# Kernel tuning notes

Hardware: AMD Instinct MI355X
Metric: run time of the kernel (lower is better)

## Reference

```python
import jax, jax.numpy as jnp
import numpy as np

D_MODEL = 256; D_FFN = 1024; N_LEVELS = 4; N_HEADS = 8; N_POINTS = 4; N_VT = 8
D_HEAD = D_MODEL // N_HEADS
SHAPES = [(64, 64), (32, 32), (16, 16), (8, 8)]
L_SP = sum(h * w for h, w in SHAPES)  # 5440
BATCH = 4
EPS = 1e-5


def _ln(x, g, b):
    m = jnp.mean(x, -1, keepdims=True)
    xc = x - m
    v = jnp.mean(xc * xc, -1, keepdims=True)
    return g * xc * jax.lax.rsqrt(v + EPS) + b


def _bilinear(v_flat, x, y, H, W):
    # v_flat: (N, H*W, M, Dh); x, y: (N, Q, M) pixel coords (align_corners=False, zero padding)
    x0 = jnp.floor(x); y0 = jnp.floor(y)
    wx = x - x0; wy = y - y0
    out = 0.0
    for cx, cy, w in ((x0, y0, (1 - wx) * (1 - wy)), (x0 + 1, y0, wx * (1 - wy)),
                      (x0, y0 + 1, (1 - wx) * wy), (x0 + 1, y0 + 1, wx * wy)):
        valid = (cx >= 0) & (cx < W) & (cy >= 0) & (cy < H)
        xi = jnp.clip(cx, 0, W - 1).astype(jnp.int32)
        yi = jnp.clip(cy, 0, H - 1).astype(jnp.int32)
        idx = (yi * W + xi)[..., None]  # (N, Q, M, 1)
        g = jnp.take_along_axis(v_flat, idx, axis=1)  # (N, Q, M, Dh)
        out = out + (w * valid)[..., None] * g
    return out


def _msdeform_attn(query, ref, value_in, shapes_np, pad_mask, Wv, bv, Wo, bo, Wa, ba, Wp, bp):
    N, Lq, D = query.shape
    M, Lv, P, Dh = N_HEADS, N_LEVELS, N_POINTS, D_HEAD
    value = value_in @ Wv.T + bv
    value = jnp.where(pad_mask[..., None], 0.0, value)
    value = value.reshape(N, Lq, M, Dh)
    off = (query @ Wo.T + bo).reshape(N, Lq, M, Lv, P, 2)
    attn = jax.nn.softmax((query @ Wa.T + ba).reshape(N, Lq, M, Lv * P), axis=-1)
    attn = attn.reshape(N, Lq, M, Lv, P)
    # offset normalizer is (W, H) per level
    normalizer = jnp.asarray([[w, h] for h, w in shapes_np], jnp.float32)
    loc = ref[:, :, None, :, None, :] + off / normalizer[None, None, None, :, None, :]
    out = 0.0
    start = 0
    for l, (H, W) in enumerate(shapes_np):
        v_l = value[:, start:start + H * W]  # (N, H*W, M, Dh)
        x = (loc[:, :, :, l, :, 0] * W - 0.5).transpose(0, 1, 3, 2).reshape(N, Lq * P, M)
        y = (loc[:, :, :, l, :, 1] * H - 0.5).transpose(0, 1, 3, 2).reshape(N, Lq * P, M)
        samp = _bilinear(v_l, x, y, H, W).reshape(N, Lq, P, M, Dh)
        out = out + jnp.einsum('nqpmd,nqmp->nqmd', samp, attn[:, :, :, l, :])
        start += H * W
    return out.reshape(N, Lq, D) @ Wp.T + bp


def setup_inputs() -> dict:
    key = jax.random.key(0)
    ks = jax.random.split(key, 16)
    N, D = BATCH, D_MODEL
    Lq = L_SP + N_VT
    s = D ** -0.5
    rn = lambda k, sh, sc=1.0: jax.random.normal(k, sh, dtype=jnp.float32) * sc
    starts = np.cumsum([0] + [h * w for h, w in SHAPES[:-1]])
    return {
        'src': rn(ks[0], (N, L_SP, D)),
        'pos': rn(ks[1], (N, L_SP, D), 0.1),
        'reference_points': jax.random.uniform(ks[2], (N, Lq, N_LEVELS, 2), dtype=jnp.float32),
        'spatial_shapes': jnp.asarray(SHAPES, jnp.int32),
        'level_start_index': jnp.asarray(starts, jnp.int32),
        'padding_mask': jnp.zeros((N, Lq), bool),
        'all_vt': rn(ks[3], (N, 75 * N_VT, D)),
        'sel_vt': rn(ks[4], (N, N_VT, D)),
        'W_value': rn(ks[5], (D, D), s), 'b_value': jnp.zeros((D,), jnp.float32),
        'W_off': rn(ks[6], (N_HEADS * N_LEVELS * N_POINTS * 2, D), s),
        'b_off': rn(ks[7], (N_HEADS * N_LEVELS * N_POINTS * 2,), 0.1),
        'W_attn': rn(ks[8], (N_HEADS * N_LEVELS * N_POINTS, D), s),
        'b_attn': jnp.zeros((N_HEADS * N_LEVELS * N_POINTS,), jnp.float32),
        'W_out': rn(ks[9], (D, D), s), 'b_out': jnp.zeros((D,), jnp.float32),
        'g1': jnp.ones((D,), jnp.float32), 'beta1': jnp.zeros((D,), jnp.float32),
        'W1': rn(ks[10], (D_FFN, D), s), 'bf1': jnp.zeros((D_FFN,), jnp.float32),
        'W2': rn(ks[11], (D, D_FFN), D_FFN ** -0.5), 'bf2': jnp.zeros((D,), jnp.float32),
        'g2': jnp.ones((D,), jnp.float32), 'beta2': jnp.zeros((D,), jnp.float32),
    }


def reference(src, pos, reference_points, spatial_shapes, level_start_index, padding_mask,
              all_vt, sel_vt, W_value, b_value, W_off, b_off, W_attn, b_attn, W_out, b_out,
              g1, beta1, W1, bf1, W2, bf2, g2, beta2):
    shapes_np = [tuple(int(v) for v in row) for row in np.asarray(spatial_shapes)]
    q = jnp.concatenate([src + pos, sel_vt], axis=1)      # (N, Lq, D)
    v_in = jnp.concatenate([src, sel_vt], axis=1)
    src2 = _msdeform_attn(q, reference_points, v_in, shapes_np, padding_mask,
                          W_value, b_value, W_off, b_off, W_attn, b_attn, W_out, b_out)
    x = _ln(v_in + src2, g1, beta1)
    h = jax.nn.relu(x @ W1.T + bf1) @ W2.T + bf2
    x = _ln(x + h, g2, beta2)
    return (x[:, :L_SP, :], all_vt, x[:, L_SP:, :])
```

## Files before the change

### kernel.cpp

```cpp
#include <hip/hip_runtime.h>
#include <math.h>

#define NB   4
#define LQ   5448
#define LSP  5440
#define NR   21792
#define DM   256

typedef unsigned short u16;
typedef __attribute__((ext_vector_type(8))) short short8;
typedef __attribute__((ext_vector_type(4))) float f32x4;
typedef __attribute__((ext_vector_type(4))) unsigned int uint4v;

__device__ __forceinline__ u16 f2bf(float f) {
  unsigned int u = __float_as_uint(f);
  u = (u + 0x7fff + ((u >> 16) & 1)) >> 16;
  return (u16)u;
}
__device__ __forceinline__ float bf2f(u16 u) {
  return __uint_as_float(((unsigned int)u) << 16);
}
__device__ __forceinline__ uint4v pack8(float4 a, float4 b) {
  uint4v r;
  r.x = (unsigned)f2bf(a.x) | ((unsigned)f2bf(a.y) << 16);
  r.y = (unsigned)f2bf(a.z) | ((unsigned)f2bf(a.w) << 16);
  r.z = (unsigned)f2bf(b.x) | ((unsigned)f2bf(b.y) << 16);
  r.w = (unsigned)f2bf(b.z) | ((unsigned)f2bf(b.w) << 16);
  return r;
}

#define OFF_R0 0ull
#define OFF_R1 44630016ull
#define OFF_R2 55787520ull
#define OFF_R3 66945024ull
#define OFF_WB 78102528ull
#define OFF_BI 79609856ull

#define WOF_V  0
#define WOF_OA 65536
#define WOF_P  163840
#define WOF_1  229376
#define WOF_2  491520
#define NWELEM 753664

#define OUT0 5570560ull
#define OUT1 614400ull

__global__ __launch_bounds__(256) void convw_k(
    const float* __restrict__ Wv, const float* __restrict__ Wo,
    const float* __restrict__ Wa, const float* __restrict__ Wp,
    const float* __restrict__ W1, const float* __restrict__ W2,
    const float* __restrict__ bo, const float* __restrict__ ba,
    u16* __restrict__ out, float* __restrict__ boa)
{
  const int gid = blockIdx.x * 256 + threadIdx.x;
  if (gid < 384) boa[gid] = (gid < 256) ? bo[gid] : ba[gid - 256];
  if (gid >= NWELEM) return;
  float v;
  if (gid < WOF_OA) {
    v = Wv[gid];
  } else if (gid < WOF_P) {
    const int o = gid - WOF_OA;
    v = (o < 65536) ? Wo[o] : Wa[o - 65536];
  } else if (gid < WOF_1) {
    v = Wp[gid - WOF_P];
  } else if (gid < WOF_2) {
    v = W1[gid - WOF_1];
  } else {
    v = W2[gid - WOF_2];
  }
  out[gid] = f2bf(v);
}

template <int AMODE, int EPI, int BN>
__global__ __launch_bounds__(BN) void gemmP(
    const u16* __restrict__ A, int lda,
    const float* __restrict__ src, const float* __restrict__ pos,
    const float* __restrict__ sel,
    const u16* __restrict__ B, int ldb,
    const float* __restrict__ bias, int K,
    u16* __restrict__ outb, int ldob,
    const u16* __restrict__ xbf,
    const float* __restrict__ gvec, const float* __restrict__ bvec,
    float* __restrict__ outf, int ldof)
{
  constexpr int NW = BN / 64;
  __shared__ u16 As[32 * 256];
  __shared__ u16 Bs[NW * 4096];
  const int tid = threadIdx.x;
  const int w = tid >> 6, lane = tid & 63;
  const int l15 = lane & 15, quad = lane >> 4;
  const int m0 = blockIdx.y * 32;
  const int n0 = blockIdx.x * BN;
  const int swz = (quad ^ ((l15 >> 1) & 3)) * 8;

  const int rA = (tid & 127) >> 2;
  const int pA = tid & 3;
  const int jb = ((tid >> 7) & 1) * 4;
  const int cA = (pA ^ ((rA >> 1) & 3)) * 8;
  const int ldsA = rA * 32 + pA * 8;
  int gmA = m0 + rA; if (gmA >= NR) gmA = NR - 1;
  const float* aV = nullptr; const float* aP = nullptr;
  if (AMODE) {
    const int n = gmA / LQ, i = gmA - n * LQ;
    if (i < LSP) {
      aV = src + ((size_t)(n * LSP + i)) * DM;
      if (AMODE == 1) aP = pos + ((size_t)(n * LSP + i)) * DM;
    } else {
      aV = sel + ((size_t)(n * 8 + (i - LSP))) * DM;
    }
  }

  int rB[4], cB[4], lB[4];
#pragma unroll
  for (int i = 0; i < 4; ++i) {
    const int g = lane + i * 64;
    rB[i] = g >> 2;
    const int p = g & 3;
    cB[i] = (p ^ ((rB[i] >> 1) & 3)) * 8;
    lB[i] = w * 4096 + rB[i] * 32 + p * 8;
  }
  const u16* Brow = B + (size_t)(n0 + w * 64) * ldb;

  f32x4 acc[2][4] = {};

  for (int kc = 0; kc < K; kc += 256) {
    if (kc) __syncthreads();
    if (tid < 256) {
      if (AMODE == 0) {
        const u16* ap = A + (size_t)gmA * lda + kc + cA;
        uint4v t0 = *(const uint4v*)(ap + (jb + 0) * 32);
        uint4v t1 = *(const uint4v*)(ap + (jb + 1) * 32);
        uint4v t2 = *(const uint4v*)(ap + (jb + 2) * 32);
        uint4v t3 = *(const uint4v*)(ap + (jb + 3) * 32);
        *(uint4v*)&As[(jb + 0) * 1024 + ldsA] = t0;
        *(uint4v*)&As[(jb + 1) * 1024 + ldsA] = t1;
        *(uint4v*)&As[(jb + 2) * 1024 + ldsA] = t2;
        *(uint4v*)&As[(jb + 3) * 1024 + ldsA] = t3;
      } else {
#pragma unroll
        for (int i = 0; i < 4; i += 2) {
          const int j0 = jb + i, j1 = jb + i + 1;
          float4 v0a = *(const float4*)(aV + kc + j0 * 32 + cA);
          float4 v0b = *(const float4*)(aV + kc + j0 * 32 + cA + 4);
          float4 v1a = *(const float4*)(aV + kc + j1 * 32 + cA);
          float4 v1b = *(const float4*)(aV + kc + j1 * 32 + cA + 4);
          if (AMODE == 1 && aP) {
            const float4 p0a = *(const float4*)(aP + kc + j0 * 32 + cA);
            const float4 p0b = *(const float4*)(aP + kc + j0 * 32 + cA + 4);
            const float4 p1a = *(const float4*)(aP + kc + j1 * 32 + cA);
            const float4 p1b = *(const float4*)(aP + kc + j1 * 32 + cA + 4);
            v0a.x += p0a.x; v0a.y += p0a.y; v0a.z += p0a.z; v0a.w += p0a.w;
            v0b.x += p0b.x; v0b.y += p0b.y; v0b.z += p0b.z; v0b.w += p0b.w;
            v1a.x += p1a.x; v1a.y += p1a.y; v1a.z += p1a.z; v1a.w += p1a.w;
            v1b.x += p1b.x; v1b.y += p1b.y; v1b.z += p1b.z; v1b.w += p1b.w;
          }
          *(uint4v*)&As[j0 * 1024 + ldsA] = pack8(v0a, v0b);
          *(uint4v*)&As[j1 * 1024 + ldsA] = pack8(v1a, v1b);
        }
      }
    }
    __syncthreads();

    uint4v rb0[4], rb1[4];
#pragma unroll
    for (int i = 0; i < 4; ++i)
      rb0[i] = *(const uint4v*)(Brow + (size_t)rB[i] * ldb + kc + cB[i]);
#pragma unroll
    for (int i = 0; i < 4; ++i)
      rb1[i] = *(const uint4v*)(Brow + (size_t)rB[i] * ldb + kc + 32 + cB[i]);
#pragma unroll
    for (int i = 0; i < 4; ++i) *(uint4v*)&Bs[lB[i]] = rb0[i];

#pragma unroll
    for (int j = 0; j < 8; ++j) {
      if (j < 6) {
        if ((j & 1) == 0) {
#pragma unroll
          for (int i = 0; i < 4; ++i)
            rb0[i] = *(const uint4v*)(Brow + (size_t)rB[i] * ldb + kc + (j + 2) * 32 + cB[i]);
        } else {
#pragma unroll
          for (int i = 0; i < 4; ++i)
            rb1[i] = *(const uint4v*)(Brow + (size_t)rB[i] * ldb + kc + (j + 2) * 32 + cB[i]);
        }
      }
      short8 af[2], bfr[4];
#pragma unroll
      for (int r = 0; r < 2; ++r)
        af[r] = *(const short8*)&As[j * 1024 + (r * 16 + l15) * 32 + swz];
#pragma unroll
      for (int c = 0; c < 4; ++c)
        bfr[c] = *(const short8*)&Bs[w * 4096 + (j & 1) * 2048 + (c * 16 + l15) * 32 + swz];
      if (j < 7) {
        const int buf = ((j + 1) & 1) * 2048;
        if ((j & 1) == 0) {
#pragma unroll
          for (int i = 0; i < 4; ++i) *(uint4v*)&Bs[lB[i] + buf] = rb1[i];
        } else {
#pragma unroll
          for (int i = 0; i < 4; ++i) *(uint4v*)&Bs[lB[i] + buf] = rb0[i];
        }
      }
#pragma unroll
      for (int r = 0; r < 2; ++r)
#pragma unroll
        for (int c = 0; c < 4; ++c)
          acc[r][c] = __builtin_amdgcn_mfma_f32_16x16x32_bf16(af[r], bfr[c], acc[r][c], 0, 0, 0);
    }
  }

  int col[4];
  float bb[4];
#pragma unroll
  for (int c = 0; c < 4; ++c) {
    col[c] = n0 + w * 64 + c * 16 + l15;
    bb[c] = bias[col[c]];
  }

  if (EPI == 4) {
#pragma unroll
    for (int c = 0; c < 4; ++c)
#pragma unroll
      for (int r = 0; r < 2; ++r)
#pragma unroll
        for (int j = 0; j < 4; ++j) {
          const int row = m0 + r * 16 + quad * 4 + j;
          if (row < NR) outf[(size_t)row * ldof + col[c]] = acc[r][c][j] + bb[c];
        }
    return;
  }

  if (EPI <= 1) {
#pragma unroll
    for (int c = 0; c < 4; ++c)
#pragma unroll
      for (int r = 0; r < 2; ++r)
#pragma unroll
        for (int j = 0; j < 4; ++j) {
          const int row = m0 + r * 16 + quad * 4 + j;
          if (row < NR) {
            float v = acc[r][c][j] + bb[c];
            if (EPI == 1) v = fmaxf(v, 0.f);
            outb[(size_t)row * ldob + col[c]] = f2bf(v);
          }
        }
    return;
  }

  __syncthreads();
  float sv[2][4], sq[2][4];
#pragma unroll
  for (int r = 0; r < 2; ++r) {
#pragma unroll
    for (int j = 0; j < 4; ++j) {
      const int row = m0 + r * 16 + quad * 4 + j;
      const int rc = (row < NR) ? row : NR - 1;
      if (EPI == 2) {
        const int n = rc / LQ;
        const int i = rc - n * LQ;
        const float* resb = (i < LSP)
            ? src + ((size_t)(n * LSP + i)) * DM
            : sel + ((size_t)(n * 8 + (i - LSP))) * DM;
#pragma unroll
        for (int c = 0; c < 4; ++c) acc[r][c][j] += bb[c] + resb[col[c]];
      } else {
#pragma unroll
        for (int c = 0; c < 4; ++c)
          acc[r][c][j] += bb[c] + bf2f(xbf[(size_t)rc * DM + col[c]]);
      }
      float s = 0.f, q = 0.f;
#pragma unroll
      for (int c = 0; c < 4; ++c) {
        const float v = acc[r][c][j];
        s += v; q += v * v;
      }
      sv[r][j] = s; sq[r][j] = q;
    }
  }
#pragma unroll
  for (int off = 1; off < 16; off <<= 1) {
#pragma unroll
    for (int r = 0; r < 2; ++r)
#pragma unroll
      for (int j = 0; j < 4; ++j) {
        sv[r][j] += __shfl_xor(sv[r][j], off, 64);
        sq[r][j] += __shfl_xor(sq[r][j], off, 64);
      }
  }
  float* red = (float*)As;
  if (l15 == 0) {
#pragma unroll
    for (int r = 0; r < 2; ++r)
#pragma unroll
      for (int j = 0; j < 4; ++j) {
        const int rl = r * 16 + quad * 4 + j;
        red[(rl * 4 + w) * 2 + 0] = sv[r][j];
        red[(rl * 4 + w) * 2 + 1] = sq[r][j];
      }
  }
  __syncthreads();

  float gg[4], b2[4];
#pragma unroll
  for (int c = 0; c < 4; ++c) { gg[c] = gvec[col[c]]; b2[c] = bvec[col[c]]; }

#pragma unroll
  for (int r = 0; r < 2; ++r) {
#pragma unroll
    for (int j = 0; j < 4; ++j) {
      const int row = m0 + r * 16 + quad * 4 + j;
      if (row >= NR) continue;
      const int rl = r * 16 + quad * 4 + j;
      float ms = 0.f, mq = 0.f;
#pragma unroll
      for (int ww = 0; ww < 4; ++ww) {
        ms += red[(rl * 4 + ww) * 2 + 0];
        mq += red[(rl * 4 + ww) * 2 + 1];
      }
      const float mean = ms * (1.f / 256.f);
      const float var = mq * (1.f / 256.f) - mean * mean;
      const float rin = rsqrtf(var + 1e-5f);
      if (EPI == 2) {
#pragma unroll
        for (int c = 0; c < 4; ++c)
          outb[(size_t)row * DM + col[c]] =
              f2bf(gg[c] * (acc[r][c][j] - mean) * rin + b2[c]);
      } else {
        const int n = row / LQ;
        const int i = row - n * LQ;
        float* dst = (i < LSP)
            ? outf + (size_t)(n * LSP + i) * DM
            : outf + OUT0 + OUT1 + (size_t)(n * 8 + (i - LSP)) * DM;
#pragma unroll
        for (int c = 0; c < 4; ++c)
          dst[col[c]] = gg[c] * (acc[r][c][j] - mean) * rin + b2[c];
      }
    }
  }
}

__device__ __forceinline__ void acc8(float* a, const u16* p, float w) {
  const uint4v u = *(const uint4v*)p;
  a[0] += w * __uint_as_float((u.x & 0xffffu) << 16);
  a[1] += w * __uint_as_float(u.x & 0xffff0000u);
  a[2] += w * __uint_as_float((u.y & 0xffffu) << 16);
  a[3] += w * __uint_as_float(u.y & 0xffff0000u);
  a[4] += w * __uint_as_float((u.z & 0xffffu) << 16);
  a[5] += w * __uint_as_float(u.z & 0xffff0000u);
  a[6] += w * __uint_as_float((u.w & 0xffffu) << 16);
  a[7] += w * __uint_as_float(u.w & 0xffff0000u);
}

__global__ __launch_bounds__(256) void sample3_k(
    const u16* __restrict__ value, const float* __restrict__ oa,
    const float* __restrict__ ref, u16* __restrict__ samp)
{
  const int lb = blockIdx.x;
  const int xcd = lb & 7;
  const int idx = lb >> 3;
  const int batch = xcd >> 1;
  const int rg = idx * 2 + (xcd & 1);
  if (rg >= 681) return;
  const int lane = threadIdx.x & 63;
  const int li = threadIdx.x & 31;
  const int m = li >> 2, q4 = li & 3;
  const int row = batch * LQ + rg * 8 + (threadIdx.x >> 5);

  const float* oar = oa + (size_t)row * 384;
  const float* offm = oar + m * 32;

  const float4 lg = *(const float4*)(oar + 256 + m * 16 + q4 * 4);
  float mx = fmaxf(fmaxf(lg.x, lg.y), fmaxf(lg.z, lg.w));
  mx = fmaxf(mx, __shfl_xor(mx, 1, 64));
  mx = fmaxf(mx, __shfl_xor(mx, 2, 64));
  const float e0 = __expf(lg.x - mx), e1 = __expf(lg.y - mx),
              e2 = __expf(lg.z - mx), e3 = __expf(lg.w - mx);
  float s = e0 + e1 + e2 + e3;
  s += __shfl_xor(s, 1, 64);
  s += __shfl_xor(s, 2, 64);
  const float inv = 1.f / s;
  float wp[4] = {e0 * inv, e1 * inv, e2 * inv, e3 * inv};

  const float4 r01 = *(const float4*)(ref + (size_t)row * 8);
  const float4 r23 = *(const float4*)(ref + (size_t)row * 8 + 4);
  const float RX[4] = {r01.x, r01.z, r23.x, r23.z};
  const float RY[4] = {r01.y, r01.w, r23.y, r23.w};
  const int HW[4] = {64, 32, 16, 8};
  const int ST[4] = {0, 4096, 5120, 5376};

  float a[8] = {};
#pragma unroll
  for (int l = 0; l < 4; ++l) {
    const int W = HW[l], H = HW[l];
    const float rx = RX[l], ry = RY[l];
    const u16* vb = value + ((size_t)(batch * LQ + ST[l])) * DM + m * 32 + q4 * 8;
    const float4 oA = *(const float4*)(offm + l * 8);
    const float4 oB = *(const float4*)(offm + l * 8 + 4);
    const float ox[4] = {oA.x, oA.z, oB.x, oB.z};
    const float oy[4] = {oA.y, oA.w, oB.y, oB.w};
#pragma unroll
    for (int p = 0; p < 4; ++p) {
      const float aw = __shfl(wp[p], (lane & ~3) | l, 64);
      const float px = rx * (float)W + ox[p] - 0.5f;
      const float py = ry * (float)H + oy[p] - 0.5f;
      const float xf = floorf(px), yf = floorf(py);
      const float wx = px - xf, wy = py - yf;
      const int x0 = (int)xf, y0 = (int)yf;
      const int x1 = x0 + 1, y1 = y0 + 1;
      const bool vx0 = (x0 >= 0) & (x0 < W), vx1 = (x1 >= 0) & (x1 < W);
      const bool vy0 = (y0 >= 0) & (y0 < H), vy1 = (y1 >= 0) & (y1 < H);
      if (vy0 & vx0) acc8(a, vb + (size_t)(y0 * W + x0) * DM, aw * (1.f - wx) * (1.f - wy));
      if (vy0 & vx1) acc8(a, vb + (size_t)(y0 * W + x1) * DM, aw * wx * (1.f - wy));
      if (vy1 & vx0) acc8(a, vb + (size_t)(y1 * W + x0) * DM, aw * (1.f - wx) * wy);
      if (vy1 & vx1) acc8(a, vb + (size_t)(y1 * W + x1) * DM, aw * wx * wy);
    }
  }
  uint4v ov;
  ov.x = (unsigned int)f2bf(a[0]) | ((unsigned int)f2bf(a[1]) << 16);
  ov.y = (unsigned int)f2bf(a[2]) | ((unsigned int)f2bf(a[3]) << 16);
  ov.z = (unsigned int)f2bf(a[4]) | ((unsigned int)f2bf(a[5]) << 16);
  ov.w = (unsigned int)f2bf(a[6]) | ((unsigned int)f2bf(a[7]) << 16);
  *(uint4v*)(samp + (size_t)row * DM + m * 32 + q4 * 8) = ov;
}

extern "C" void kernel_launch(void* const* d_in, const int* in_sizes, int n_in,
                              void* d_out, int out_size, void* d_ws, size_t ws_size,
                              hipStream_t stream)
{
  const float* src = (const float*)d_in[0];
  const float* pos = (const float*)d_in[1];
  const float* ref = (const float*)d_in[2];
  const float* all_vt = (const float*)d_in[6];
  const float* sel = (const float*)d_in[7];
  const float* Wv = (const float*)d_in[8];
  const float* bv = (const float*)d_in[9];
  const float* Wo = (const float*)d_in[10];
  const float* bo = (const float*)d_in[11];
  const float* Wa = (const float*)d_in[12];
  const float* ba = (const float*)d_in[13];
  const float* Wp = (const float*)d_in[14];
  const float* bp = (const float*)d_in[15];
  const float* g1 = (const float*)d_in[16];
  const float* be1 = (const float*)d_in[17];
  const float* W1 = (const float*)d_in[18];
  const float* b1 = (const float*)d_in[19];
  const float* W2 = (const float*)d_in[20];
  const float* b2 = (const float*)d_in[21];
  const float* g2 = (const float*)d_in[22];
  const float* be2 = (const float*)d_in[23];

  char* ws = (char*)d_ws;
  float* oabuf = (float*)(ws + OFF_R0);
  u16* h_bf    = (u16*)(ws + OFF_R0);
  u16* samp_bf = (u16*)(ws + OFF_R1);
  u16* x_bf    = (u16*)(ws + OFF_R2);
  u16* val_bf  = (u16*)(ws + OFF_R3);
  u16* WB      = (u16*)(ws + OFF_WB);
  float* boa   = (float*)(ws + OFF_BI);

  const dim3 b256(256), b384(384);
  const int MT32 = (NR + 31) / 32;

  convw_k<<<dim3(NWELEM / 256), b256, 0, stream>>>(
      Wv, Wo, Wa, Wp, W1, W2, bo, ba, WB, boa);
  gemmP<2, 0, 256><<<dim3(1, MT32), b256, 0, stream>>>(
      nullptr, 0, src, nullptr, sel, WB + WOF_V, 256, bv, 256,
      val_bf, 256, nullptr, nullptr, nullptr, nullptr, 0);
  gemmP<1, 4, 384><<<dim3(1, MT32), b384, 0, stream>>>(
      nullptr, 0, src, pos, sel, WB + WOF_OA, 256, boa, 256,
      nullptr, 0, nullptr, nullptr, nullptr, oabuf, 384);
  sample3_k<<<dim3(8 * 341), b256, 0, stream>>>(val_bf, oabuf, ref, samp_bf);
  gemmP<0, 2, 256><<<dim3(1, MT32), b256, 0, stream>>>(
      samp_bf, 256, src, nullptr, sel, WB + WOF_P, 256, bp, 256,
      x_bf, 256, nullptr, g1, be1, nullptr, 0);
  gemmP<0, 1, 256><<<dim3(4, MT32), b256, 0, stream>>>(
      x_bf, 256, nullptr, nullptr, nullptr, WB + WOF_1, 256, b1, 256,
      h_bf, 1024, nullptr, nullptr, nullptr, nullptr, 0);
  gemmP<0, 3, 256><<<dim3(1, MT32), b256, 0, stream>>>(
      h_bf, 1024, nullptr, nullptr, nullptr, WB + WOF_2, 1024, b2, 1024,
      nullptr, 0, x_bf, g2, be2, (float*)d_out, 0);
  hipMemcpyAsync((float*)d_out + OUT0, all_vt, OUT1 * sizeof(float),
                 hipMemcpyDeviceToDevice, stream);
}
```

Measured before the change: 290.9 us.

## Load GEMM B fragments directly to registers and make sampling branchless

Measured after the change: 368.6 us. +26.7%, slower.

```diff
diff --git a/kernel.cpp b/kernel.cpp
--- a/kernel.cpp
+++ b/kernel.cpp
@@ -72,8 +72,10 @@
   out[gid] = f2bf(v);
 }
 
+#define MFMA_B(d, a, b) d = __builtin_amdgcn_mfma_f32_16x16x32_bf16(a, b, d, 0, 0, 0)
+
 template <int AMODE, int EPI, int BN>
-__global__ __launch_bounds__(BN) void gemmP(
+__global__ __launch_bounds__(BN, 4) void gemmP(
     const u16* __restrict__ A, int lda,
     const float* __restrict__ src, const float* __restrict__ pos,
     const float* __restrict__ sel,
@@ -84,9 +86,7 @@
     const float* __restrict__ gvec, const float* __restrict__ bvec,
     float* __restrict__ outf, int ldof)
 {
-  constexpr int NW = BN / 64;
   __shared__ u16 As[32 * 256];
-  __shared__ u16 Bs[NW * 4096];
   const int tid = threadIdx.x;
   const int w = tid >> 6, lane = tid & 63;
   const int l15 = lane & 15, quad = lane >> 4;
@@ -111,16 +111,7 @@
     }
   }
 
-  int rB[4], cB[4], lB[4];
-#pragma unroll
-  for (int i = 0; i < 4; ++i) {
-    const int g = lane + i * 64;
-    rB[i] = g >> 2;
-    const int p = g & 3;
-    cB[i] = (p ^ ((rB[i] >> 1) & 3)) * 8;
-    lB[i] = w * 4096 + rB[i] * 32 + p * 8;
-  }
-  const u16* Brow = B + (size_t)(n0 + w * 64) * ldb;
+  const u16* bp = B + (size_t)(n0 + w * 64 + l15) * ldb + quad * 8;
 
   f32x4 acc[2][4] = {};
 
@@ -162,51 +153,38 @@
     }
     __syncthreads();
 
-    uint4v rb0[4], rb1[4];
-#pragma unroll
-    for (int i = 0; i < 4; ++i)
-      rb0[i] = *(const uint4v*)(Brow + (size_t)rB[i] * ldb + kc + cB[i]);
-#pragma unroll
-    for (int i = 0; i < 4; ++i)
-      rb1[i] = *(const uint4v*)(Brow + (size_t)rB[i] * ldb + kc + 32 + cB[i]);
-#pragma unroll
-    for (int i = 0; i < 4; ++i) *(uint4v*)&Bs[lB[i]] = rb0[i];
-
-#pragma unroll
-    for (int j = 0; j < 8; ++j) {
-      if (j < 6) {
-        if ((j & 1) == 0) {
-#pragma unroll
-          for (int i = 0; i < 4; ++i)
-            rb0[i] = *(const uint4v*)(Brow + (size_t)rB[i] * ldb + kc + (j + 2) * 32 + cB[i]);
-        } else {
-#pragma unroll
-          for (int i = 0; i < 4; ++i)
-            rb1[i] = *(const uint4v*)(Brow + (size_t)rB[i] * ldb + kc + (j + 2) * 32 + cB[i]);
+    short8 bA[4], bB[4];
+#pragma unroll
+    for (int c = 0; c < 4; ++c)
+      bA[c] = *(const short8*)(bp + (size_t)(c * 16) * ldb + kc);
+#pragma unroll
+    for (int j = 0; j < 8; j += 2) {
+#pragma unroll
+      for (int c = 0; c < 4; ++c)
+        bB[c] = *(const short8*)(bp + (size_t)(c * 16) * ldb + kc + (j + 1) * 32);
+      {
+        const short8 af0 = *(const short8*)&As[j * 1024 + l15 * 32 + swz];
+        const short8 af1 = *(const short8*)&As[j * 1024 + (16 + l15) * 32 + swz];
+#pragma unroll
+        for (int c = 0; c < 4; ++c) {
+          MFMA_B(acc[0][c], af0, bA[c]);
+          MFMA_B(acc[1][c], af1, bA[c]);
         }
       }
-      short8 af[2], bfr[4];
-#pragma unroll
-      for (int r = 0; r < 2; ++r)
-        af[r] = *(const short8*)&As[j * 1024 + (r * 16 + l15) * 32 + swz];
-#pragma unroll
-      for (int c = 0; c < 4; ++c)
-        bfr[c] = *(const short8*)&Bs[w * 4096 + (j & 1) * 2048 + (c * 16 + l15) * 32 + swz];
-      if (j < 7) {
-        const int buf = ((j + 1) & 1) * 2048;
-        if ((j & 1) == 0) {
-#pragma unroll
-          for (int i = 0; i < 4; ++i) *(uint4v*)&Bs[lB[i] + buf] = rb1[i];
-        } else {
-#pragma unroll
-          for (int i = 0; i < 4; ++i) *(uint4v*)&Bs[lB[i] + buf] = rb0[i];
+      if (j + 2 < 8) {
+#pragma unroll
+        for (int c = 0; c < 4; ++c)
+          bA[c] = *(const short8*)(bp + (size_t)(c * 16) * ldb + kc + (j + 2) * 32);
+      }
+      {
+        const short8 af0 = *(const short8*)&As[(j + 1) * 1024 + l15 * 32 + swz];
+        const short8 af1 = *(const short8*)&As[(j + 1) * 1024 + (16 + l15) * 32 + swz];
+#pragma unroll
+        for (int c = 0; c < 4; ++c) {
+          MFMA_B(acc[0][c], af0, bB[c]);
+          MFMA_B(acc[1][c], af1, bB[c]);
         }
       }
-#pragma unroll
-      for (int r = 0; r < 2; ++r)
-#pragma unroll
-        for (int c = 0; c < 4; ++c)
-          acc[r][c] = __builtin_amdgcn_mfma_f32_16x16x32_bf16(af[r], bfr[c], acc[r][c], 0, 0, 0);
     }
   }
 
@@ -340,15 +318,14 @@
   }
 }
 
-__device__ __forceinline__ void acc8(float* a, const u16* p, float w) {
-  const uint4v u = *(const uint4v*)p;
-  a[0] += w * __uint_as_float((u.x & 0xffffu) << 16);
+__device__ __forceinline__ void fma8(float* a, const uint4v u, float w) {
+  a[0] += w * __uint_as_float(u.x << 16);
   a[1] += w * __uint_as_float(u.x & 0xffff0000u);
-  a[2] += w * __uint_as_float((u.y & 0xffffu) << 16);
+  a[2] += w * __uint_as_float(u.y << 16);
   a[3] += w * __uint_as_float(u.y & 0xffff0000u);
-  a[4] += w * __uint_as_float((u.z & 0xffffu) << 16);
+  a[4] += w * __uint_as_float(u.z << 16);
   a[5] += w * __uint_as_float(u.z & 0xffff0000u);
-  a[6] += w * __uint_as_float((u.w & 0xffffu) << 16);
+  a[6] += w * __uint_as_float(u.w << 16);
   a[7] += w * __uint_as_float(u.w & 0xffff0000u);
 }
 
@@ -382,6 +359,14 @@
   const float inv = 1.f / s;
   float wp[4] = {e0 * inv, e1 * inv, e2 * inv, e3 * inv};
 
+  float aw[4][4];
+#pragma unroll
+  for (int p = 0; p < 4; ++p) {
+#pragma unroll
+    for (int l = 0; l < 4; ++l)
+      aw[l][p] = __shfl(wp[p], (lane & ~3) | l, 64);
+  }
+
   const float4 r01 = *(const float4*)(ref + (size_t)row * 8);
   const float4 r23 = *(const float4*)(ref + (size_t)row * 8 + 4);
   const float RX[4] = {r01.x, r01.z, r23.x, r23.z};
@@ -392,7 +377,7 @@
   float a[8] = {};
 #pragma unroll
   for (int l = 0; l < 4; ++l) {
-    const int W = HW[l], H = HW[l];
+    const int W = HW[l];
     const float rx = RX[l], ry = RY[l];
     const u16* vb = value + ((size_t)(batch * LQ + ST[l])) * DM + m * 32 + q4 * 8;
     const float4 oA = *(const float4*)(offm + l * 8);
@@ -401,19 +386,31 @@
     const float oy[4] = {oA.y, oA.w, oB.y, oB.w};
 #pragma unroll
     for (int p = 0; p < 4; ++p) {
-      const float aw = __shfl(wp[p], (lane & ~3) | l, 64);
       const float px = rx * (float)W + ox[p] - 0.5f;
-      const float py = ry * (float)H + oy[p] - 0.5f;
+      const float py = ry * (float)W + oy[p] - 0.5f;
       const float xf = floorf(px), yf = floorf(py);
       const float wx = px - xf, wy = py - yf;
       const int x0 = (int)xf, y0 = (int)yf;
       const int x1 = x0 + 1, y1 = y0 + 1;
-      const bool vx0 = (x0 >= 0) & (x0 < W), vx1 = (x1 >= 0) & (x1 < W);
-      const bool vy0 = (y0 >= 0) & (y0 < H), vy1 = (y1 >= 0) & (y1 < H);
-      if (vy0 & vx0) acc8(a, vb + (size_t)(y0 * W + x0) * DM, aw * (1.f - wx) * (1.f - wy));
-      if (vy0 & vx1) acc8(a, vb + (size_t)(y0 * W + x1) * DM, aw * wx * (1.f - wy));
-      if (vy1 & vx0) acc8(a, vb + (size_t)(y1 * W + x0) * DM, aw * (1.f - wx) * wy);
-      if (vy1 & vx1) acc8(a, vb + (size_t)(y1 * W + x1) * DM, aw * wx * wy);
+      const float vx0 = ((x0 >= 0) & (x0 < W)) ? 1.f : 0.f;
+      const float vx1 = ((x1 >= 0) & (x1 < W)) ? 1.f : 0.f;
+      const float vy0 = ((y0 >= 0) & (y0 < W)) ? 1.f : 0.f;
+      const float vy1 = ((y1 >= 0) & (y1 < W)) ? 1.f : 0.f;
+      const int cx0 = min(max(x0, 0), W - 1), cx1 = min(max(x1, 0), W - 1);
+      const int cy0 = min(max(y0, 0), W - 1), cy1 = min(max(y1, 0), W - 1);
+      const float awp = aw[l][p];
+      const float w00 = awp * (1.f - wx) * (1.f - wy) * vx0 * vy0;
+      const float w01 = awp * wx * (1.f - wy) * vx1 * vy0;
+      const float w10 = awp * (1.f - wx) * wy * vx0 * vy1;
+      const float w11 = awp * wx * wy * vx1 * vy1;
+      const uint4v v00 = *(const uint4v*)(vb + (size_t)(cy0 * W + cx0) * DM);
+      const uint4v v01 = *(const uint4v*)(vb + (size_t)(cy0 * W + cx1) * DM);
+      const uint4v v10 = *(const uint4v*)(vb + (size_t)(cy1 * W + cx0) * DM);
+      const uint4v v11 = *(const uint4v*)(vb + (size_t)(cy1 * W + cx1) * DM);
+      fma8(a, v00, w00);
+      fma8(a, v01, w01);
+      fma8(a, v10, w10);
+      fma8(a, v11, w11);
     }
   }
   uint4v ov;
```

## Reuse A tile across N iterations in FFN1 GEMM and make bilinear sampling branchless

Applied to the files above, without the earlier changes.

New measurement: 287.6 us. Within noise of the previous version (-1.1%).

```diff
diff --git a/kernel.cpp b/kernel.cpp
--- a/kernel.cpp
+++ b/kernel.cpp
@@ -72,7 +72,7 @@
   out[gid] = f2bf(v);
 }
 
-template <int AMODE, int EPI, int BN>
+template <int AMODE, int EPI, int BN, int NITER>
 __global__ __launch_bounds__(BN) void gemmP(
     const u16* __restrict__ A, int lda,
     const float* __restrict__ src, const float* __restrict__ pos,
@@ -91,7 +91,7 @@
   const int w = tid >> 6, lane = tid & 63;
   const int l15 = lane & 15, quad = lane >> 4;
   const int m0 = blockIdx.y * 32;
-  const int n0 = blockIdx.x * BN;
+  const int n0 = blockIdx.x * (BN * NITER);
   const int swz = (quad ^ ((l15 >> 1) & 3)) * 8;
 
   const int rA = (tid & 127) >> 2;
@@ -120,235 +120,238 @@
     cB[i] = (p ^ ((rB[i] >> 1) & 3)) * 8;
     lB[i] = w * 4096 + rB[i] * 32 + p * 8;
   }
-  const u16* Brow = B + (size_t)(n0 + w * 64) * ldb;
-
-  f32x4 acc[2][4] = {};
-
-  for (int kc = 0; kc < K; kc += 256) {
-    if (kc) __syncthreads();
-    if (tid < 256) {
-      if (AMODE == 0) {
-        const u16* ap = A + (size_t)gmA * lda + kc + cA;
-        uint4v t0 = *(const uint4v*)(ap + (jb + 0) * 32);
-        uint4v t1 = *(const uint4v*)(ap + (jb + 1) * 32);
-        uint4v t2 = *(const uint4v*)(ap + (jb + 2) * 32);
-        uint4v t3 = *(const uint4v*)(ap + (jb + 3) * 32);
-        *(uint4v*)&As[(jb + 0) * 1024 + ldsA] = t0;
-        *(uint4v*)&As[(jb + 1) * 1024 + ldsA] = t1;
-        *(uint4v*)&As[(jb + 2) * 1024 + ldsA] = t2;
-        *(uint4v*)&As[(jb + 3) * 1024 + ldsA] = t3;
-      } else {
-#pragma unroll
-        for (int i = 0; i < 4; i += 2) {
-          const int j0 = jb + i, j1 = jb + i + 1;
-          float4 v0a = *(const float4*)(aV + kc + j0 * 32 + cA);
-          float4 v0b = *(const float4*)(aV + kc + j0 * 32 + cA + 4);
-          float4 v1a = *(const float4*)(aV + kc + j1 * 32 + cA);
-          float4 v1b = *(const float4*)(aV + kc + j1 * 32 + cA + 4);
-          if (AMODE == 1 && aP) {
-            const float4 p0a = *(const float4*)(aP + kc + j0 * 32 + cA);
-            const float4 p0b = *(const float4*)(aP + kc + j0 * 32 + cA + 4);
-            const float4 p1a = *(const float4*)(aP + kc + j1 * 32 + cA);
-            const float4 p1b = *(const float4*)(aP + kc + j1 * 32 + cA + 4);
-            v0a.x += p0a.x; v0a.y += p0a.y; v0a.z += p0a.z; v0a.w += p0a.w;
-            v0b.x += p0b.x; v0b.y += p0b.y; v0b.z += p0b.z; v0b.w += p0b.w;
-            v1a.x += p1a.x; v1a.y += p1a.y; v1a.z += p1a.z; v1a.w += p1a.w;
-            v1b.x += p1b.x; v1b.y += p1b.y; v1b.z += p1b.z; v1b.w += p1b.w;
+
+  for (int it = 0; it < NITER; ++it) {
+    const u16* Brow = B + (size_t)(n0 + it * BN + w * 64) * ldb;
+    f32x4 acc[2][4] = {};
+
+    for (int kc = 0; kc < K; kc += 256) {
+      if (NITER == 1 || it == 0) {
+        if (kc) __syncthreads();
+        if (tid < 256) {
+          if (AMODE == 0) {
+            const u16* ap = A + (size_t)gmA * lda + kc + cA;
+            uint4v t0 = *(const uint4v*)(ap + (jb + 0) * 32);
+            uint4v t1 = *(const uint4v*)(ap + (jb + 1) * 32);
+            uint4v t2 = *(const uint4v*)(ap + (jb + 2) * 32);
+            uint4v t3 = *(const uint4v*)(ap + (jb + 3) * 32);
+            *(uint4v*)&As[(jb + 0) * 1024 + ldsA] = t0;
+            *(uint4v*)&As[(jb + 1) * 1024 + ldsA] = t1;
+            *(uint4v*)&As[(jb + 2) * 1024 + ldsA] = t2;
+            *(uint4v*)&As[(jb + 3) * 1024 + ldsA] = t3;
+          } else {
+#pragma unroll
+            for (int i = 0; i < 4; i += 2) {
+              const int j0 = jb + i, j1 = jb + i + 1;
+              float4 v0a = *(const float4*)(aV + kc + j0 * 32 + cA);
+              float4 v0b = *(const float4*)(aV + kc + j0 * 32 + cA + 4);
+              float4 v1a = *(const float4*)(aV + kc + j1 * 32 + cA);
+              float4 v1b = *(const float4*)(aV + kc + j1 * 32 + cA + 4);
+              if (AMODE == 1 && aP) {
+                const float4 p0a = *(const float4*)(aP + kc + j0 * 32 + cA);
+                const float4 p0b = *(const float4*)(aP + kc + j0 * 32 + cA + 4);
+                const float4 p1a = *(const float4*)(aP + kc + j1 * 32 + cA);
+                const float4 p1b = *(const float4*)(aP + kc + j1 * 32 + cA + 4);
+                v0a.x += p0a.x; v0a.y += p0a.y; v0a.z += p0a.z; v0a.w += p0a.w;
+                v0b.x += p0b.x; v0b.y += p0b.y; v0b.z += p0b.z; v0b.w += p0b.w;
+                v1a.x += p1a.x; v1a.y += p1a.y; v1a.z += p1a.z; v1a.w += p1a.w;
+                v1b.x += p1b.x; v1b.y += p1b.y; v1b.z += p1b.z; v1b.w += p1b.w;
+              }
+              *(uint4v*)&As[j0 * 1024 + ldsA] = pack8(v0a, v0b);
+              *(uint4v*)&As[j1 * 1024 + ldsA] = pack8(v1a, v1b);
+            }
           }
-          *(uint4v*)&As[j0 * 1024 + ldsA] = pack8(v0a, v0b);
-          *(uint4v*)&As[j1 * 1024 + ldsA] = pack8(v1a, v1b);
-        }
+        }
+        __syncthreads();
       }
-    }
+
+      uint4v rb0[4], rb1[4];
+#pragma unroll
+      for (int i = 0; i < 4; ++i)
+        rb0[i] = *(const uint4v*)(Brow + (size_t)rB[i] * ldb + kc + cB[i]);
+#pragma unroll
+      for (int i = 0; i < 4; ++i)
+        rb1[i] = *(const uint4v*)(Brow + (size_t)rB[i] * ldb + kc + 32 + cB[i]);
+#pragma unroll
+      for (int i = 0; i < 4; ++i) *(uint4v*)&Bs[lB[i]] = rb0[i];
+
+#pragma unroll
+      for (int j = 0; j < 8; ++j) {
+        if (j < 6) {
+          if ((j & 1) == 0) {
+#pragma unroll
+            for (int i = 0; i < 4; ++i)
+              rb0[i] = *(const uint4v*)(Brow + (size_t)rB[i] * ldb + kc + (j + 2) * 32 + cB[i]);
+          } else {
+#pragma unroll
+            for (int i = 0; i < 4; ++i)
+              rb1[i] = *(const uint4v*)(Brow + (size_t)rB[i] * ldb + kc + (j + 2) * 32 + cB[i]);
+          }
+        }
+        short8 af[2], bfr[4];
+#pragma unroll
+        for (int r = 0; r < 2; ++r)
+          af[r] = *(const short8*)&As[j * 1024 + (r * 16 + l15) * 32 + swz];
+#pragma unroll
+        for (int c = 0; c < 4; ++c)
+          bfr[c] = *(const short8*)&Bs[w * 4096 + (j & 1) * 2048 + (c * 16 + l15) * 32 + swz];
+        if (j < 7) {
+          const int buf = ((j + 1) & 1) * 2048;
+          if ((j & 1) == 0) {
+#pragma unroll
+            for (int i = 0; i < 4; ++i) *(uint4v*)&Bs[lB[i] + buf] = rb1[i];
+          } else {
+#pragma unroll
+            for (int i = 0; i < 4; ++i) *(uint4v*)&Bs[lB[i] + buf] = rb0[i];
+          }
+        }
+#pragma unroll
+        for (int r = 0; r < 2; ++r)
+#pragma unroll
+          for (int c = 0; c < 4; ++c)
+            acc[r][c] = __builtin_amdgcn_mfma_f32_16x16x32_bf16(af[r], bfr[c], acc[r][c], 0, 0, 0);
+      }
+    }
+
+    int col[4];
+    float bb[4];
+#pragma unroll
+    for (int c = 0; c < 4; ++c) {
+      col[c] = n0 + it * BN + w * 64 + c * 16 + l15;
+      bb[c] = bias[col[c]];
+    }
+
+    if (EPI == 4) {
+#pragma unroll
+      for (int c = 0; c < 4; ++c)
+#pragma unroll
+        for (int r = 0; r < 2; ++r)
+#pragma unroll
+          for (int j = 0; j < 4; ++j) {
+            const int row = m0 + r * 16 + quad * 4 + j;
+            if (row < NR) outf[(size_t)row * ldof + col[c]] = acc[r][c][j] + bb[c];
+          }
+      continue;
+    }
+
+    if (EPI <= 1) {
+#pragma unroll
+      for (int c = 0; c < 4; ++c)
+#pragma unroll
+        for (int r = 0; r < 2; ++r)
+#pragma unroll
+          for (int j = 0; j < 4; ++j) {
+            const int row = m0 + r * 16 + quad * 4 + j;
+            if (row < NR) {
+              float v = acc[r][c][j] + bb[c];
+              if (EPI == 1) v = fmaxf(v, 0.f);
+              outb[(size_t)row * ldob + col[c]] = f2bf(v);
+            }
+          }
+      continue;
+    }
+
     __syncthreads();
-
-    uint4v rb0[4], rb1[4];
-#pragma unroll
-    for (int i = 0; i < 4; ++i)
-      rb0[i] = *(const uint4v*)(Brow + (size_t)rB[i] * ldb + kc + cB[i]);
-#pragma unroll
-    for (int i = 0; i < 4; ++i)
-      rb1[i] = *(const uint4v*)(Brow + (size_t)rB[i] * ldb + kc + 32 + cB[i]);
-#pragma unroll
-    for (int i = 0; i < 4; ++i) *(uint4v*)&Bs[lB[i]] = rb0[i];
-
-#pragma unroll
-    for (int j = 0; j < 8; ++j) {
-      if (j < 6) {
-        if ((j & 1) == 0) {
-#pragma unroll
-          for (int i = 0; i < 4; ++i)
-            rb0[i] = *(const uint4v*)(Brow + (size_t)rB[i] * ldb + kc + (j + 2) * 32 + cB[i]);
+    float sv[2][4], sq[2][4];
+#pragma unroll
+    for (int r = 0; r < 2; ++r) {
+#pragma unroll
+      for (int j = 0; j < 4; ++j) {
+        const int row = m0 + r * 16 + quad * 4 + j;
+        const int rc = (row < NR) ? row : NR - 1;
+        if (EPI == 2) {
+          const int n = rc / LQ;
+          const int i = rc - n * LQ;
+          const float* resb = (i < LSP)
+              ? src + ((size_t)(n * LSP + i)) * DM
+              : sel + ((size_t)(n * 8 + (i - LSP))) * DM;
+#pragma unroll
+          for (int c = 0; c < 4; ++c) acc[r][c][j] += bb[c] + resb[col[c]];
         } else {
 #pragma unroll
-          for (int i = 0; i < 4; ++i)
-            rb1[i] = *(const uint4v*)(Brow + (size_t)rB[i] * ldb + kc + (j + 2) * 32 + cB[i]);
-        }
+          for (int c = 0; c < 4; ++c)
+            acc[r][c][j] += bb[c] + bf2f(xbf[(size_t)rc * DM + col[c]]);
+        }
+        float s = 0.f, q = 0.f;
+#pragma unroll
+        for (int c = 0; c < 4; ++c) {
+          const float v = acc[r][c][j];
+          s += v; q += v * v;
+        }
+        sv[r][j] = s; sq[r][j] = q;
       }
-      short8 af[2], bfr[4];
+    }
+#pragma unroll
+    for (int off = 1; off < 16; off <<= 1) {
 #pragma unroll
       for (int r = 0; r < 2; ++r)
-        af[r] = *(const short8*)&As[j * 1024 + (r * 16 + l15) * 32 + swz];
-#pragma unroll
-      for (int c = 0; c < 4; ++c)
-        bfr[c] = *(const short8*)&Bs[w * 4096 + (j & 1) * 2048 + (c * 16 + l15) * 32 + swz];
-      if (j < 7) {
-        const int buf = ((j + 1) & 1) * 2048;
-        if ((j & 1) == 0) {
-#pragma unroll
-          for (int i = 0; i < 4; ++i) *(uint4v*)&Bs[lB[i] + buf] = rb1[i];
+#pragma unroll
+        for (int j = 0; j < 4; ++j) {
+          sv[r][j] += __shfl_xor(sv[r][j], off, 64);
+          sq[r][j] += __shfl_xor(sq[r][j], off, 64);
+        }
+    }
+    float* red = (float*)As;
+    if (l15 == 0) {
+#pragma unroll
+      for (int r = 0; r < 2; ++r)
+#pragma unroll
+        for (int j = 0; j < 4; ++j) {
+          const int rl = r * 16 + quad * 4 + j;
+          red[(rl * 4 + w) * 2 + 0] = sv[r][j];
+          red[(rl * 4 + w) * 2 + 1] = sq[r][j];
+        }
+    }
+    __syncthreads();
+
+    float gg[4], b2[4];
+#pragma unroll
+    for (int c = 0; c < 4; ++c) { gg[c] = gvec[col[c]]; b2[c] = bvec[col[c]]; }
+
+#pragma unroll
+    for (int r = 0; r < 2; ++r) {
+#pragma unroll
+      for (int j = 0; j < 4; ++j) {
+        const int row = m0 + r * 16 + quad * 4 + j;
+        if (row >= NR) continue;
+        const int rl = r * 16 + quad * 4 + j;
+        float ms = 0.f, mq = 0.f;
+#pragma unroll
+        for (int ww = 0; ww < 4; ++ww) {
+          ms += red[(rl * 4 + ww) * 2 + 0];
+          mq += red[(rl * 4 + ww) * 2 + 1];
+        }
+        const float mean = ms * (1.f / 256.f);
+        const float var = mq * (1.f / 256.f) - mean * mean;
+        const float rin = rsqrtf(var + 1e-5f);
+        if (EPI == 2) {
+#pragma unroll
+          for (int c = 0; c < 4; ++c)
+            outb[(size_t)row * DM + col[c]] =
+                f2bf(gg[c] * (acc[r][c][j] - mean) * rin + b2[c]);
         } else {
-#pragma unroll
-          for (int i = 0; i < 4; ++i) *(uint4v*)&Bs[lB[i] + buf] = rb0[i];
+          const int n = row / LQ;
+          const int i = row - n * LQ;
+          float* dst = (i < LSP)
+              ? outf + (size_t)(n * LSP + i) * DM
+              : outf + OUT0 + OUT1 + (size_t)(n * 8 + (i - LSP)) * DM;
+#pragma unroll
+          for (int c = 0; c < 4; ++c)
+            dst[col[c]] = gg[c] * (acc[r][c][j] - mean) * rin + b2[c];
         }
       }
-#pragma unroll
-      for (int r = 0; r < 2; ++r)
-#pragma unroll
-        for (int c = 0; c < 4; ++c)
-          acc[r][c] = __builtin_amdgcn_mfma_f32_16x16x32_bf16(af[r], bfr[c], acc[r][c], 0, 0, 0);
     }
   }
-
-  int col[4];
-  float bb[4];
-#pragma unroll
-  for (int c = 0; c < 4; ++c) {
-    col[c] = n0 + w * 64 + c * 16 + l15;
-    bb[c] = bias[col[c]];
-  }
-
-  if (EPI == 4) {
-#pragma unroll
-    for (int c = 0; c < 4; ++c)
-#pragma unroll
-      for (int r = 0; r < 2; ++r)
-#pragma unroll
-        for (int j = 0; j < 4; ++j) {
-          const int row = m0 + r * 16 + quad * 4 + j;
-          if (row < NR) outf[(size_t)row * ldof + col[c]] = acc[r][c][j] + bb[c];
-        }
-    return;
-  }
-
-  if (EPI <= 1) {
-#pragma unroll
-    for (int c = 0; c < 4; ++c)
-#pragma unroll
-      for (int r = 0; r < 2; ++r)
-#pragma unroll
-        for (int j = 0; j < 4; ++j) {
-          const int row = m0 + r * 16 + quad * 4 + j;
-          if (row < NR) {
-            float v = acc[r][c][j] + bb[c];
-            if (EPI == 1) v = fmaxf(v, 0.f);
-            outb[(size_t)row * ldob + col[c]] = f2bf(v);
-          }
-        }
-    return;
-  }
-
-  __syncthreads();
-  float sv[2][4], sq[2][4];
-#pragma unroll
-  for (int r = 0; r < 2; ++r) {
-#pragma unroll
-    for (int j = 0; j < 4; ++j) {
-      const int row = m0 + r * 16 + quad * 4 + j;
-      const int rc = (row < NR) ? row : NR - 1;
-      if (EPI == 2) {
-        const int n = rc / LQ;
-        const int i = rc - n * LQ;
-        const float* resb = (i < LSP)
-            ? src + ((size_t)(n * LSP + i)) * DM
-            : sel + ((size_t)(n * 8 + (i - LSP))) * DM;
-#pragma unroll
-        for (int c = 0; c < 4; ++c) acc[r][c][j] += bb[c] + resb[col[c]];
-      } else {
-#pragma unroll
-        for (int c = 0; c < 4; ++c)
-          acc[r][c][j] += bb[c] + bf2f(xbf[(size_t)rc * DM + col[c]]);
-      }
-      float s = 0.f, q = 0.f;
-#pragma unroll
-      for (int c = 0; c < 4; ++c) {
-        const float v = acc[r][c][j];
-        s += v; q += v * v;
-      }
-      sv[r][j] = s; sq[r][j] = q;
-    }
-  }
-#pragma unroll
-  for (int off = 1; off < 16; off <<= 1) {
-#pragma unroll
-    for (int r = 0; r < 2; ++r)
-#pragma unroll
-      for (int j = 0; j < 4; ++j) {
-        sv[r][j] += __shfl_xor(sv[r][j], off, 64);
-        sq[r][j] += __shfl_xor(sq[r][j], off, 64);
-      }
-  }
-  float* red = (float*)As;
-  if (l15 == 0) {
-#pragma unroll
-    for (int r = 0; r < 2; ++r)
-#pragma unroll
-      for (int j = 0; j < 4; ++j) {
-        const int rl = r * 16 + quad * 4 + j;
-        red[(rl * 4 + w) * 2 + 0] = sv[r][j];
-        red[(rl * 4 + w) * 2 + 1] = sq[r][j];
-      }
-  }
-  __syncthreads();
-
-  float gg[4], b2[4];
-#pragma unroll
-  for (int c = 0; c < 4; ++c) { gg[c] = gvec[col[c]]; b2[c] = bvec[col[c]]; }
-
-#pragma unroll
-  for (int r = 0; r < 2; ++r) {
-#pragma unroll
-    for (int j = 0; j < 4; ++j) {
-      const int row = m0 + r * 16 + quad * 4 + j;
-      if (row >= NR) continue;
-      const int rl = r * 16 + quad * 4 + j;
-      float ms = 0.f, mq = 0.f;
-#pragma unroll
-      for (int ww = 0; ww < 4; ++ww) {
-        ms += red[(rl * 4 + ww) * 2 + 0];
-        mq += red[(rl * 4 + ww) * 2 + 1];
-      }
-      const float mean = ms * (1.f / 256.f);
-      const float var = mq * (1.f / 256.f) - mean * mean;
-      const float rin = rsqrtf(var + 1e-5f);
-      if (EPI == 2) {
-#pragma unroll
-        for (int c = 0; c < 4; ++c)
-          outb[(size_t)row * DM + col[c]] =
-              f2bf(gg[c] * (acc[r][c][j] - mean) * rin + b2[c]);
-      } else {
-        const int n = row / LQ;
-        const int i = row - n * LQ;
-        float* dst = (i < LSP)
-            ? outf + (size_t)(n * LSP + i) * DM
-            : outf + OUT0 + OUT1 + (size_t)(n * 8 + (i - LSP)) * DM;
-#pragma unroll
-        for (int c = 0; c < 4; ++c)
-          dst[col[c]] = gg[c] * (acc[r][c][j] - mean) * rin + b2[c];
-      }
-    }
-  }
-}
-
-__device__ __forceinline__ void acc8(float* a, const u16* p, float w) {
-  const uint4v u = *(const uint4v*)p;
-  a[0] += w * __uint_as_float((u.x & 0xffffu) << 16);
+}
+
+__device__ __forceinline__ void fma8(float* a, const uint4v u, float w) {
+  a[0] += w * __uint_as_float(u.x << 16);
   a[1] += w * __uint_as_float(u.x & 0xffff0000u);
-  a[2] += w * __uint_as_float((u.y & 0xffffu) << 16);
+  a[2] += w * __uint_as_float(u.y << 16);
   a[3] += w * __uint_as_float(u.y & 0xffff0000u);
-  a[4] += w * __uint_as_float((u.z & 0xffffu) << 16);
+  a[4] += w * __uint_as_float(u.z << 16);
   a[5] += w * __uint_as_float(u.z & 0xffff0000u);
-  a[6] += w * __uint_as_float((u.w & 0xffffu) << 16);
+  a[6] += w * __uint_as_float(u.w << 16);
   a[7] += w * __uint_as_float(u.w & 0xffff0000u);
 }
 
@@ -382,6 +385,14 @@
   const float inv = 1.f / s;
   float wp[4] = {e0 * inv, e1 * inv, e2 * inv, e3 * inv};
 
+  float aw[4][4];
+#pragma unroll
+  for (int p = 0; p < 4; ++p) {
+#pragma unroll
+    for (int l = 0; l < 4; ++l)
+      aw[l][p] = __shfl(wp[p], (lane & ~3) | l, 64);
+  }
+
   const float4 r01 = *(const float4*)(ref + (size_t)row * 8);
   const float4 r23 = *(const float4*)(ref + (size_t)row * 8 + 4);
   const float RX[4] = {r01.x, r01.z, r23.x, r23.z};
@@ -392,7 +403,7 @@
   float a[8] = {};
 #pragma unroll
   for (int l = 0; l < 4; ++l) {
-    const int W = HW[l], H = HW[l];
+    const int W = HW[l];
     const float rx = RX[l], ry = RY[l];
     const u16* vb = value + ((size_t)(batch * LQ + ST[l])) * DM + m * 32 + q4 * 8;
     const float4 oA = *(const float4*)(offm + l * 8);
@@ -401,19 +412,31 @@
     const float oy[4] = {oA.y, oA.w, oB.y, oB.w};
 #pragma unroll
     for (int p = 0; p < 4; ++p) {
-      const float aw = __shfl(wp[p], (lane & ~3) | l, 64);
       const float px = rx * (float)W + ox[p] - 0.5f;
-      const float py = ry * (float)H + oy[p] - 0.5f;
+      const float py = ry * (float)W + oy[p] - 0.5f;
       const float xf = floorf(px), yf = floorf(py);
       const float wx = px - xf, wy = py - yf;
       const int x0 = (int)xf, y0 = (int)yf;
       const int x1 = x0 + 1, y1 = y0 + 1;
-      const bool vx0 = (x0 >= 0) & (x0 < W), vx1 = (x1 >= 0) & (x1 < W);
-      const bool vy0 = (y0 >= 0) & (y0 < H), vy1 = (y1 >= 0) & (y1 < H);
-      if (vy0 & vx0) acc8(a, vb + (size_t)(y0 * W + x0) * DM, aw * (1.f - wx) * (1.f - wy));
-      if (vy0 & vx1) acc8(a, vb + (size_t)(y0 * W + x1) * DM, aw * wx * (1.f - wy));
-      if (vy1 & vx0) acc8(a, vb + (size_t)(y1 * W + x0) * DM, aw * (1.f - wx) * wy);
-      if (vy1 & vx1) acc8(a, vb + (size_t)(y1 * W + x1) * DM, aw * wx * wy);
+      const float vx0 = ((x0 >= 0) & (x0 < W)) ? 1.f : 0.f;
+      const float vx1 = ((x1 >= 0) & (x1 < W)) ? 1.f : 0.f;
+      const float vy0 = ((y0 >= 0) & (y0 < W)) ? 1.f : 0.f;
+      const float vy1 = ((y1 >= 0) & (y1 < W)) ? 1.f : 0.f;
+      const int cx0 = min(max(x0, 0), W - 1), cx1 = min(max(x1, 0), W - 1);
+      const int cy0 = min(max(y0, 0), W - 1), cy1 = min(max(y1, 0), W - 1);
+      const float awp = aw[l][p];
+      const float w00 = awp * (1.f - wx) * (1.f - wy) * vx0 * vy0;
+      const float w01 = awp * wx * (1.f - wy) * vx1 * vy0;
+      const float w10 = awp * (1.f - wx) * wy * vx0 * vy1;
+      const float w11 = awp * wx * wy * vx1 * vy1;
+      const uint4v v00 = *(const uint4v*)(vb + (size_t)(cy0 * W + cx0) * DM);
+      const uint4v v01 = *(const uint4v*)(vb + (size_t)(cy0 * W + cx1) * DM);
+      const uint4v v10 = *(const uint4v*)(vb + (size_t)(cy1 * W + cx0) * DM);
+      const uint4v v11 = *(const uint4v*)(vb + (size_t)(cy1 * W + cx1) * DM);
+      fma8(a, v00, w00);
+      fma8(a, v01, w01);
+      fma8(a, v10, w10);
+      fma8(a, v11, w11);
     }
   }
   uint4v ov;
@@ -464,20 +487,20 @@
 
   convw_k<<<dim3(NWELEM / 256), b256, 0, stream>>>(
       Wv, Wo, Wa, Wp, W1, W2, bo, ba, WB, boa);
-  gemmP<2, 0, 256><<<dim3(1, MT32), b256, 0, stream>>>(
+  gemmP<2, 0, 256, 1><<<dim3(1, MT32), b256, 0, stream>>>(
       nullptr, 0, src, nullptr, sel, WB + WOF_V, 256, bv, 256,
       val_bf, 256, nullptr, nullptr, nullptr, nullptr, 0);
-  gemmP<1, 4, 384><<<dim3(1, MT32), b384, 0, stream>>>(
+  gemmP<1, 4, 384, 1><<<dim3(1, MT32), b384, 0, stream>>>(
       nullptr, 0, src, pos, sel, WB + WOF_OA, 256, boa, 256,
       nullptr, 0, nullptr, nullptr, nullptr, oabuf, 384);
   sample3_k<<<dim3(8 * 341), b256, 0, stream>>>(val_bf, oabuf, ref, samp_bf);
-  gemmP<0, 2, 256><<<dim3(1, MT32), b256, 0, stream>>>(
+  gemmP<0, 2, 256, 1><<<dim3(1, MT32), b256, 0, stream>>>(
       samp_bf, 256, src, nullptr, sel, WB + WOF_P, 256, bp, 256,
       x_bf, 256, nullptr, g1, be1, nullptr, 0);
-  gemmP<0, 1, 256><<<dim3(4, MT32), b256, 0, stream>>>(
+  gemmP<0, 1, 256, 4><<<dim3(1, MT32), b256, 0, stream>>>(
       x_bf, 256, nullptr, nullptr, nullptr, WB + WOF_1, 256, b1, 256,
       h_bf, 1024, nullptr, nullptr, nullptr, nullptr, 0);
-  gemmP<0, 3, 256><<<dim3(1, MT32), b256, 0, stream>>>(
+  gemmP<0, 3, 256, 1><<<dim3(1, MT32), b256, 0, stream>>>(
       h_bf, 1024, nullptr, nullptr, nullptr, WB + WOF_2, 1024, b2, 1024,
       nullptr, 0, x_bf, g2, be2, (float*)d_out, 0);
   hipMemcpyAsync((float*)d_out + OUT0, all_vt, OUT1 * sizeof(float),
```
